# Kernel optimization log

Hardware: AMD Instinct MI355X
Metric: run time of the kernel (lower is better)

## Reference

```python
import jax, jax.numpy as jnp
import numpy as np

V, E, H, A, L = 32000, 512, 1024, 512, 2  # vocab, embed, hidden, attn, n_layers
B, S = 64, 128


def setup_inputs() -> dict:
    key = jax.random.key(0)
    ks = jax.random.split(key, 20)
    sc = 0.02
    inp = {
        "token": jax.random.randint(ks[0], (B,), 0, V),
        "hidden": jax.random.normal(ks[1], (L, B, H), jnp.float32),
        "cell": jax.random.normal(ks[2], (L, B, H), jnp.float32),
        "enc_out": jax.random.normal(ks[3], (S, B, 2 * H), jnp.float32),
        "emb_table": (jax.random.normal(ks[4], (V, E), jnp.float32) * sc).at[0].set(0.0),  # padding_idx=0
        "W_enc": jax.random.normal(ks[5], (A, 2 * H), jnp.float32) * sc,
        "W_dec": jax.random.normal(ks[6], (A, H), jnp.float32) * sc,
        "v_w": jax.random.normal(ks[7], (A,), jnp.float32) * sc,
        "W_ih0": jax.random.normal(ks[8], (4 * H, E + 2 * H), jnp.float32) * sc,
        "W_hh0": jax.random.normal(ks[9], (4 * H, H), jnp.float32) * sc,
        "b_ih0": jax.random.normal(ks[10], (4 * H,), jnp.float32) * sc,
        "b_hh0": jax.random.normal(ks[11], (4 * H,), jnp.float32) * sc,
        "W_ih1": jax.random.normal(ks[12], (4 * H, H), jnp.float32) * sc,
        "W_hh1": jax.random.normal(ks[13], (4 * H, H), jnp.float32) * sc,
        "b_ih1": jax.random.normal(ks[14], (4 * H,), jnp.float32) * sc,
        "b_hh1": jax.random.normal(ks[15], (4 * H,), jnp.float32) * sc,
        "fc_W": jax.random.normal(ks[16], (V, 3 * H), jnp.float32) * sc,
        "fc_b": jax.random.normal(ks[17], (V,), jnp.float32) * sc,
    }
    return inp


def _lstm_cell(x, h, c, W_ih, W_hh, b_ih, b_hh):
    # PyTorch gate order: i, f, g, o
    gates = x @ W_ih.T + h @ W_hh.T + (b_ih + b_hh)  # (B, 4H)
    i, f, g, o = jnp.split(gates, 4, axis=-1)
    i, f, o = jax.nn.sigmoid(i), jax.nn.sigmoid(f), jax.nn.sigmoid(o)
    c_new = f * c + i * jnp.tanh(g)
    h_new = o * jnp.tanh(c_new)
    return h_new, c_new


def reference(token, hidden, cell, enc_out, emb_table, W_enc, W_dec, v_w,
              W_ih0, W_hh0, b_ih0, b_hh0, W_ih1, W_hh1, b_ih1, b_hh1, fc_W, fc_b):
    embedded = emb_table[token]                      # (B, E)
    top = hidden[-1]                                 # (B, H)
    enc_t = jnp.transpose(enc_out, (1, 0, 2))        # (B, S, 2H)
    # additive attention: v . tanh(W_enc enc + W_dec s_t)
    energy = jnp.tanh(jnp.einsum('bsd,ad->bsa', enc_t, W_enc)
                      + (top @ W_dec.T)[:, None, :])  # (B, S, A)
    score = jnp.einsum('bsa,a->bs', energy, v_w)     # (B, S)
    alpha = jax.nn.softmax(score, axis=-1)           # (B, S)
    context = jnp.einsum('bs,bsd->bd', alpha, enc_t)  # (B, 2H)
    x0 = jnp.concatenate([embedded, context], axis=-1)  # (B, E+2H)
    h0, c0 = _lstm_cell(x0, hidden[0], cell[0], W_ih0, W_hh0, b_ih0, b_hh0)
    h1, c1 = _lstm_cell(h0, hidden[1], cell[1], W_ih1, W_hh1, b_ih1, b_hh1)
    logits = jnp.concatenate([h1, context], axis=-1) @ fc_W.T + fc_b  # (B, V)
    new_hidden = jnp.stack([h0, h1], axis=0)
    new_cell = jnp.stack([c0, c1], axis=0)
    return logits, new_hidden, new_cell, alpha
```

## Files before the change

kernel.cpp:

```cpp
#include <hip/hip_runtime.h>
#include <stdint.h>

#define HD    1024
#define BATCH 64
#define SEQ   128
#define AD    512
#define EMBD  512
#define VOCAB 32000

typedef float f32x4 __attribute__((ext_vector_type(4)));
typedef short bf8   __attribute__((ext_vector_type(8)));

#define WS_SCOREP 0
#define WS_DECP   32768
#define WS_G0     65536
#define WS_G1     1114112
#define WS_X0     2162688
#define WS_XFC    2326528
#define WS_H0     2523136

#define OUT_LOGITS 0
#define OUT_HID    2048000
#define OUT_CELL   2179072
#define OUT_ALPHA  2310144

__device__ __forceinline__ short f2bf(float f) {
  uint32_t u = __float_as_uint(f);
  u += 0x7FFF + ((u >> 16) & 1);
  return (short)(u >> 16);
}

__device__ __forceinline__ void store_bf4(short* p, float4 v) {
  short4 s;
  s.x = f2bf(v.x); s.y = f2bf(v.y); s.z = f2bf(v.z); s.w = f2bf(v.w);
  *(short4*)p = s;
}

__global__ __launch_bounds__(256) void k_init(float* __restrict__ ws,
                                              const int* __restrict__ token,
                                              const float* __restrict__ emb) {
  int idx = blockIdx.x * 256 + threadIdx.x;
  int b = idx >> 7, e4 = idx & 127;
  int tok = token[b];
  float4 v = *(const float4*)&emb[(size_t)tok * EMBD + e4 * 4];
  *(float4*)&ws[WS_X0 + (size_t)b * 2560 + e4 * 4] = v;
}

__global__ __launch_bounds__(256) void gemm_thin(
    const float* __restrict__ A, int a_stride,
    const float* __restrict__ Bm,
    float* __restrict__ C, int ldc,
    const float* __restrict__ bias,
    int K_total) {
  __shared__ __align__(16) short As[64][72];
  __shared__ __align__(16) short Bs[64][72];
  const int tid = threadIdx.x;
  const int wave = tid >> 6, lane = tid & 63;
  const int quad = lane >> 4, l16 = lane & 15;
  const int n0 = blockIdx.x * 64;
  const int srow = tid >> 4, sc4 = (tid & 15) * 4;

  f32x4 acc[4];
#pragma unroll
  for (int i = 0; i < 4; ++i) acc[i] = (f32x4){0.f, 0.f, 0.f, 0.f};

  float4 pa[4], pb[4];
#pragma unroll
  for (int p = 0; p < 4; ++p) {
    int row = srow + p * 16;
    pa[p] = *(const float4*)&A[(size_t)row * a_stride + sc4];
    pb[p] = *(const float4*)&Bm[(size_t)(n0 + row) * K_total + sc4];
  }

  for (int kt = 0; kt < K_total; kt += 64) {
#pragma unroll
    for (int p = 0; p < 4; ++p) {
      int row = srow + p * 16;
      store_bf4(&As[row][sc4], pa[p]);
      store_bf4(&Bs[row][sc4], pb[p]);
    }
    __syncthreads();
    if (kt + 64 < K_total) {
      int kn = kt + 64;
#pragma unroll
      for (int p = 0; p < 4; ++p) {
        int row = srow + p * 16;
        pa[p] = *(const float4*)&A[(size_t)row * a_stride + kn + sc4];
        pb[p] = *(const float4*)&Bm[(size_t)(n0 + row) * K_total + kn + sc4];
      }
    }
#pragma unroll
    for (int kk = 0; kk < 64; kk += 32) {
      bf8 af = *(const bf8*)&As[wave * 16 + l16][kk + quad * 8];
#pragma unroll
      for (int ns = 0; ns < 4; ++ns) {
        bf8 bf = *(const bf8*)&Bs[ns * 16 + l16][kk + quad * 8];
        acc[ns] = __builtin_amdgcn_mfma_f32_16x16x32_bf16(af, bf, acc[ns], 0, 0, 0);
      }
    }
    __syncthreads();
  }

#pragma unroll
  for (int ns = 0; ns < 4; ++ns) {
    int n = n0 + ns * 16 + l16;
    float bv = bias ? bias[n] : 0.f;
#pragma unroll
    for (int r = 0; r < 4; ++r) {
      int m = wave * 16 + quad * 4 + r;
      C[(size_t)m * ldc + n] = acc[ns][r] + bv;
    }
  }
}

__global__ __launch_bounds__(256) void gemm2(
    const float* __restrict__ A1, int s1, int K1, const float* __restrict__ B1,
    const float* __restrict__ A2, int s2, int K2, const float* __restrict__ B2,
    float* __restrict__ Cslab, int tiles_pz) {
  __shared__ __align__(16) short As[64][72];
  __shared__ __align__(16) short Bs[64][72];
  const int tid = threadIdx.x;
  const int wave = tid >> 6, lane = tid & 63;
  const int quad = lane >> 4, l16 = lane & 15;
  const int n0 = blockIdx.x * 64;
  const int z = blockIdx.z;
  const int t0 = z * tiles_pz;
  const int srow = tid >> 4, sc4 = (tid & 15) * 4;

  f32x4 acc[4];
#pragma unroll
  for (int i = 0; i < 4; ++i) acc[i] = (f32x4){0.f, 0.f, 0.f, 0.f};

  float4 pa[4], pb[4];
  auto loadAB = [&](int tile) {
    int kv = tile * 64;
    const float* Ap; const float* Bp; int as, ks, ko;
    if (kv < K1) { Ap = A1; Bp = B1; as = s1; ks = K1; ko = kv; }
    else         { Ap = A2; Bp = B2; as = s2; ks = K2; ko = kv - K1; }
#pragma unroll
    for (int p = 0; p < 4; ++p) {
      int row = srow + p * 16;
      pa[p] = *(const float4*)&Ap[(size_t)row * as + ko + sc4];
      pb[p] = *(const float4*)&Bp[(size_t)(n0 + row) * ks + ko + sc4];
    }
  };

  loadAB(t0);
  for (int ti = t0; ti < t0 + tiles_pz; ++ti) {
#pragma unroll
    for (int p = 0; p < 4; ++p) {
      int row = srow + p * 16;
      store_bf4(&As[row][sc4], pa[p]);
      store_bf4(&Bs[row][sc4], pb[p]);
    }
    __syncthreads();
    if (ti + 1 < t0 + tiles_pz) loadAB(ti + 1);
#pragma unroll
    for (int kk = 0; kk < 64; kk += 32) {
      bf8 af = *(const bf8*)&As[wave * 16 + l16][kk + quad * 8];
#pragma unroll
      for (int ns = 0; ns < 4; ++ns) {
        bf8 bf = *(const bf8*)&Bs[ns * 16 + l16][kk + quad * 8];
        acc[ns] = __builtin_amdgcn_mfma_f32_16x16x32_bf16(af, bf, acc[ns], 0, 0, 0);
      }
    }
    __syncthreads();
  }

  float* C = Cslab + (size_t)z * (64 * 4096);
#pragma unroll
  for (int ns = 0; ns < 4; ++ns) {
    int n = n0 + ns * 16 + l16;
#pragma unroll
    for (int r = 0; r < 4; ++r) {
      int m = wave * 16 + quad * 4 + r;
      C[(size_t)m * 4096 + n] = acc[ns][r];
    }
  }
}

__global__ __launch_bounds__(256) void k_attn(
    const float* __restrict__ enc, const float* __restrict__ Wenc,
    const float* __restrict__ dec_proj, const float* __restrict__ vw,
    float* __restrict__ scorep) {
  __shared__ __align__(16) short As[64][72];
  __shared__ __align__(16) short Bs[128][72];
  const int tid = threadIdx.x;
  const int wave = tid >> 6, lane = tid & 63;
  const int quad = lane >> 4, l16 = lane & 15;
  const int mblk = blockIdx.x, nblk = blockIdx.y;
  const int b = mblk >> 1, s0 = (mblk & 1) * 64;
  const int n0 = nblk * 128;
  const size_t abase = ((size_t)s0 * BATCH + b) * 2048;
  const int srow = tid >> 4, sc4 = (tid & 15) * 4;

  f32x4 acc[8];
#pragma unroll
  for (int i = 0; i < 8; ++i) acc[i] = (f32x4){0.f, 0.f, 0.f, 0.f};

  float4 pa[4], pb[8];
  auto loadAB = [&](int kt) {
#pragma unroll
    for (int p = 0; p < 4; ++p) {
      int row = srow + p * 16;
      pa[p] = *(const float4*)&enc[abase + (size_t)row * (BATCH * 2048) + kt + sc4];
    }
#pragma unroll
    for (int p = 0; p < 8; ++p) {
      int row = srow + p * 16;
      pb[p] = *(const float4*)&Wenc[(size_t)(n0 + row) * 2048 + kt + sc4];
    }
  };

  loadAB(0);
  for (int kt = 0; kt < 2048; kt += 64) {
#pragma unroll
    for (int p = 0; p < 4; ++p) store_bf4(&As[srow + p * 16][sc4], pa[p]);
#pragma unroll
    for (int p = 0; p < 8; ++p) store_bf4(&Bs[srow + p * 16][sc4], pb[p]);
    __syncthreads();
    if (kt + 64 < 2048) loadAB(kt + 64);
#pragma unroll
    for (int kk = 0; kk < 64; kk += 32) {
      bf8 af = *(const bf8*)&As[wave * 16 + l16][kk + quad * 8];
#pragma unroll
      for (int ns = 0; ns < 8; ++ns) {
        bf8 bf = *(const bf8*)&Bs[ns * 16 + l16][kk + quad * 8];
        acc[ns] = __builtin_amdgcn_mfma_f32_16x16x32_bf16(af, bf, acc[ns], 0, 0, 0);
      }
    }
    __syncthreads();
  }

  float part[4] = {0.f, 0.f, 0.f, 0.f};
#pragma unroll
  for (int ns = 0; ns < 8; ++ns) {
    int n = n0 + ns * 16 + l16;
    float dp = dec_proj[b * AD + n];
    float vv = vw[n];
#pragma unroll
    for (int r = 0; r < 4; ++r) part[r] += tanhf(acc[ns][r] + dp) * vv;
  }
#pragma unroll
  for (int r = 0; r < 4; ++r) {
    float v = part[r];
    v += __shfl_xor(v, 1);
    v += __shfl_xor(v, 2);
    v += __shfl_xor(v, 4);
    v += __shfl_xor(v, 8);
    if (l16 == 0)
      scorep[nblk * (BATCH * SEQ) + mblk * 64 + wave * 16 + quad * 4 + r] = v;
  }
}

__global__ __launch_bounds__(256) void k_softmax_ctx(
    const float* __restrict__ scorep, const float* __restrict__ enc,
    float* __restrict__ alpha_out, float* __restrict__ x0,
    float* __restrict__ xfc) {
  const int b = blockIdx.x, dchunk = blockIdx.y, t = threadIdx.x;
  __shared__ float al[128];
  __shared__ float buf[128];
  float sv = 0.f;
  if (t < 128) {
    sv = scorep[b * SEQ + t] + scorep[8192 + b * SEQ + t]
       + scorep[16384 + b * SEQ + t] + scorep[24576 + b * SEQ + t];
    buf[t] = sv;
  }
  __syncthreads();
  for (int off = 64; off > 0; off >>= 1) {
    if (t < off) buf[t] = fmaxf(buf[t], buf[t + off]);
    __syncthreads();
  }
  float mx = buf[0];
  __syncthreads();
  float e = 0.f;
  if (t < 128) { e = __expf(sv - mx); buf[t] = e; }
  __syncthreads();
  for (int off = 64; off > 0; off >>= 1) {
    if (t < off) buf[t] += buf[t + off];
    __syncthreads();
  }
  float inv = 1.f / buf[0];
  if (t < 128) {
    float a = e * inv;
    al[t] = a;
    if (dchunk == 0) alpha_out[b * SEQ + t] = a;
  }
  __syncthreads();

  const int d = dchunk * 1024 + t * 4;
  float4 acc = make_float4(0.f, 0.f, 0.f, 0.f);
#pragma unroll 4
  for (int s = 0; s < SEQ; ++s) {
    float4 ev = *(const float4*)&enc[((size_t)s * BATCH + b) * 2048 + d];
    float w = al[s];
    acc.x += w * ev.x; acc.y += w * ev.y;
    acc.z += w * ev.z; acc.w += w * ev.w;
  }
  *(float4*)&x0[(size_t)b * 2560 + 512 + d] = acc;
  *(float4*)&xfc[(size_t)b * 3072 + 1024 + d] = acc;
}

__global__ __launch_bounds__(256) void k_act(
    const float* __restrict__ gslab,
    const float* __restrict__ b_ih, const float* __restrict__ b_hh,
    const float* __restrict__ cell_in,
    float* __restrict__ hid_out, float* __restrict__ cell_out,
    float* __restrict__ hdst, int hstride) {
  int idx = blockIdx.x * 256 + threadIdx.x;
  int b = idx >> 10, n = idx & 1023;
  float gi = b_ih[n]        + b_hh[n];
  float gf = b_ih[1024 + n] + b_hh[1024 + n];
  float gg = b_ih[2048 + n] + b_hh[2048 + n];
  float go = b_ih[3072 + n] + b_hh[3072 + n];
#pragma unroll
  for (int sl = 0; sl < 4; ++sl) {
    const float* g = gslab + (size_t)sl * (64 * 4096) + (size_t)b * 4096;
    gi += g[n];
    gf += g[1024 + n];
    gg += g[2048 + n];
    go += g[3072 + n];
  }
  float i = 1.f / (1.f + __expf(-gi));
  float f = 1.f / (1.f + __expf(-gf));
  float o = 1.f / (1.f + __expf(-go));
  float c = f * cell_in[idx] + i * tanhf(gg);
  float h = o * tanhf(c);
  cell_out[idx] = c;
  hid_out[idx] = h;
  hdst[(size_t)b * hstride + n] = h;
}

extern "C" void kernel_launch(void* const* d_in, const int* in_sizes, int n_in,
                              void* d_out, int out_size, void* d_ws, size_t ws_size,
                              hipStream_t stream) {
  const int*   token  = (const int*)d_in[0];
  const float* hidden = (const float*)d_in[1];
  const float* cell   = (const float*)d_in[2];
  const float* enc    = (const float*)d_in[3];
  const float* emb    = (const float*)d_in[4];
  const float* W_enc  = (const float*)d_in[5];
  const float* W_dec  = (const float*)d_in[6];
  const float* v_w    = (const float*)d_in[7];
  const float* W_ih0  = (const float*)d_in[8];
  const float* W_hh0  = (const float*)d_in[9];
  const float* b_ih0  = (const float*)d_in[10];
  const float* b_hh0  = (const float*)d_in[11];
  const float* W_ih1  = (const float*)d_in[12];
  const float* W_hh1  = (const float*)d_in[13];
  const float* b_ih1  = (const float*)d_in[14];
  const float* b_hh1  = (const float*)d_in[15];
  const float* fc_W   = (const float*)d_in[16];
  const float* fc_b   = (const float*)d_in[17];

  float* out = (float*)d_out;
  float* ws  = (float*)d_ws;

  float* scorep   = ws + WS_SCOREP;
  float* dec_proj = ws + WS_DECP;
  float* gates0   = ws + WS_G0;
  float* gates1   = ws + WS_G1;
  float* x0       = ws + WS_X0;
  float* xfc      = ws + WS_XFC;
  float* h0       = ws + WS_H0;

  k_init<<<32, 256, 0, stream>>>(ws, token, emb);

  gemm_thin<<<dim3(8, 1, 1), 256, 0, stream>>>(
      hidden + BATCH * HD, HD, W_dec, dec_proj, AD, nullptr, 1024);

  k_attn<<<dim3(128, 4), 256, 0, stream>>>(enc, W_enc, dec_proj, v_w, scorep);

  k_softmax_ctx<<<dim3(64, 2), 256, 0, stream>>>(scorep, enc, out + OUT_ALPHA, x0, xfc);

  gemm2<<<dim3(64, 1, 4), 256, 0, stream>>>(
      x0, 2560, 2560, W_ih0, hidden, HD, 1024, W_hh0, gates0, 14);

  k_act<<<256, 256, 0, stream>>>(gates0, b_ih0, b_hh0, cell,
                                 out + OUT_HID, out + OUT_CELL, h0, HD);

  gemm2<<<dim3(64, 1, 4), 256, 0, stream>>>(
      h0, HD, 1024, W_ih1, hidden + BATCH * HD, HD, 1024, W_hh1, gates1, 8);

  k_act<<<256, 256, 0, stream>>>(gates1, b_ih1, b_hh1, cell + BATCH * HD,
                                 out + OUT_HID + BATCH * HD,
                                 out + OUT_CELL + BATCH * HD, xfc, 3072);

  gemm_thin<<<dim3(500, 1, 1), 256, 0, stream>>>(
      xfc, 3072, fc_W, out + OUT_LOGITS, VOCAB, fc_b, 3072);
}
```

Baseline: 768.9 us.

## Split FC GEMM by K and overlap context part with layer-0 gates

Splits the output projection into a context half, computed together with the layer-0 gate GEMM in one launch, and an h1 half computed last that adds the stored partial result. Activations (embedding, context, hidden states, h0/h1) and W_enc are pre-converted to bf16 in workspace so GEMMs load half-width A/B operands. The dec-projection GEMM, embedding gather and conversions are merged into one prep kernel. This fills the GPU better during the small gate GEMM and shortens the serial tail. The cost is extra workspace traffic for the partial logits and the W_enc conversion on every call.

```diff
diff --git a/kernel.cpp b/kernel.cpp
--- a/kernel.cpp
+++ b/kernel.cpp
@@ -15,9 +15,12 @@
 #define WS_DECP   32768
 #define WS_G0     65536
 #define WS_G1     1114112
-#define WS_X0     2162688
-#define WS_XFC    2326528
-#define WS_H0     2523136
+#define WS_LCTX   2162688
+#define WS_X0BF   4210688
+#define WS_XFCBF  4292608
+#define WS_HIDBF  4390912
+#define WS_WENCBF 4456448
+#define WS_H0BF   4980736
 
 #define OUT_LOGITS 0
 #define OUT_HID    2048000
@@ -36,28 +39,14 @@
   *(short4*)p = s;
 }
 
-__global__ __launch_bounds__(256) void k_init(float* __restrict__ ws,
-                                              const int* __restrict__ token,
-                                              const float* __restrict__ emb) {
-  int idx = blockIdx.x * 256 + threadIdx.x;
-  int b = idx >> 7, e4 = idx & 127;
-  int tok = token[b];
-  float4 v = *(const float4*)&emb[(size_t)tok * EMBD + e4 * 4];
-  *(float4*)&ws[WS_X0 + (size_t)b * 2560 + e4 * 4] = v;
-}
-
-__global__ __launch_bounds__(256) void gemm_thin(
-    const float* __restrict__ A, int a_stride,
-    const float* __restrict__ Bm,
-    float* __restrict__ C, int ldc,
-    const float* __restrict__ bias,
-    int K_total) {
-  __shared__ __align__(16) short As[64][72];
-  __shared__ __align__(16) short Bs[64][72];
+__device__ __forceinline__ void gemm_f32A(
+    short (*As)[72], short (*Bs)[72],
+    const float* __restrict__ A, int lda,
+    const float* __restrict__ Bm, int ldb, int K_total, int n0,
+    float* __restrict__ C, int ldc, const float* __restrict__ bias) {
   const int tid = threadIdx.x;
   const int wave = tid >> 6, lane = tid & 63;
   const int quad = lane >> 4, l16 = lane & 15;
-  const int n0 = blockIdx.x * 64;
   const int srow = tid >> 4, sc4 = (tid & 15) * 4;
 
   f32x4 acc[4];
@@ -68,8 +57,8 @@
 #pragma unroll
   for (int p = 0; p < 4; ++p) {
     int row = srow + p * 16;
-    pa[p] = *(const float4*)&A[(size_t)row * a_stride + sc4];
-    pb[p] = *(const float4*)&Bm[(size_t)(n0 + row) * K_total + sc4];
+    pa[p] = *(const float4*)&A[(size_t)row * lda + sc4];
+    pb[p] = *(const float4*)&Bm[(size_t)(n0 + row) * ldb + sc4];
   }
 
   for (int kt = 0; kt < K_total; kt += 64) {
@@ -85,8 +74,8 @@
 #pragma unroll
       for (int p = 0; p < 4; ++p) {
         int row = srow + p * 16;
-        pa[p] = *(const float4*)&A[(size_t)row * a_stride + kn + sc4];
-        pb[p] = *(const float4*)&Bm[(size_t)(n0 + row) * K_total + kn + sc4];
+        pa[p] = *(const float4*)&A[(size_t)row * lda + kn + sc4];
+        pb[p] = *(const float4*)&Bm[(size_t)(n0 + row) * ldb + kn + sc4];
       }
     }
 #pragma unroll
@@ -94,8 +83,8 @@
       bf8 af = *(const bf8*)&As[wave * 16 + l16][kk + quad * 8];
 #pragma unroll
       for (int ns = 0; ns < 4; ++ns) {
-        bf8 bf = *(const bf8*)&Bs[ns * 16 + l16][kk + quad * 8];
-        acc[ns] = __builtin_amdgcn_mfma_f32_16x16x32_bf16(af, bf, acc[ns], 0, 0, 0);
+        bf8 bq = *(const bf8*)&Bs[ns * 16 + l16][kk + quad * 8];
+        acc[ns] = __builtin_amdgcn_mfma_f32_16x16x32_bf16(af, bq, acc[ns], 0, 0, 0);
       }
     }
     __syncthreads();
@@ -113,74 +102,112 @@
   }
 }
 
-__global__ __launch_bounds__(256) void gemm2(
-    const float* __restrict__ A1, int s1, int K1, const float* __restrict__ B1,
-    const float* __restrict__ A2, int s2, int K2, const float* __restrict__ B2,
-    float* __restrict__ Cslab, int tiles_pz) {
-  __shared__ __align__(16) short As[64][72];
-  __shared__ __align__(16) short Bs[64][72];
+__device__ __forceinline__ void gemm_bf16A(
+    short (*As)[72], short (*Bs)[72],
+    const short* __restrict__ A1, int lda1, int K1,
+    const float* __restrict__ B1, int ldb1,
+    const short* __restrict__ A2, int lda2,
+    const float* __restrict__ B2, int ldb2,
+    int t0, int ntiles, int n0,
+    float* __restrict__ C, int ldc,
+    const float* __restrict__ bias,
+    const float* __restrict__ Cadd, int ldadd) {
   const int tid = threadIdx.x;
   const int wave = tid >> 6, lane = tid & 63;
   const int quad = lane >> 4, l16 = lane & 15;
-  const int n0 = blockIdx.x * 64;
-  const int z = blockIdx.z;
-  const int t0 = z * tiles_pz;
-  const int srow = tid >> 4, sc4 = (tid & 15) * 4;
+  const int arow = tid >> 3, ac8 = (tid & 7) * 8;
+  const int brow = tid >> 4, bc4 = (tid & 15) * 4;
 
   f32x4 acc[4];
 #pragma unroll
   for (int i = 0; i < 4; ++i) acc[i] = (f32x4){0.f, 0.f, 0.f, 0.f};
 
-  float4 pa[4], pb[4];
+  bf8 qa[2];
+  float4 pb[4];
   auto loadAB = [&](int tile) {
     int kv = tile * 64;
-    const float* Ap; const float* Bp; int as, ks, ko;
-    if (kv < K1) { Ap = A1; Bp = B1; as = s1; ks = K1; ko = kv; }
-    else         { Ap = A2; Bp = B2; as = s2; ks = K2; ko = kv - K1; }
-#pragma unroll
-    for (int p = 0; p < 4; ++p) {
-      int row = srow + p * 16;
-      pa[p] = *(const float4*)&Ap[(size_t)row * as + ko + sc4];
-      pb[p] = *(const float4*)&Bp[(size_t)(n0 + row) * ks + ko + sc4];
-    }
+    const short* Ap; const float* Bp; int la, lb, ko;
+    if (kv < K1) { Ap = A1; Bp = B1; la = lda1; lb = ldb1; ko = kv; }
+    else         { Ap = A2; Bp = B2; la = lda2; lb = ldb2; ko = kv - K1; }
+#pragma unroll
+    for (int p = 0; p < 2; ++p)
+      qa[p] = *(const bf8*)&Ap[(size_t)(arow + p * 32) * la + ko + ac8];
+#pragma unroll
+    for (int p = 0; p < 4; ++p)
+      pb[p] = *(const float4*)&Bp[(size_t)(n0 + brow + p * 16) * lb + ko + bc4];
   };
 
   loadAB(t0);
-  for (int ti = t0; ti < t0 + tiles_pz; ++ti) {
-#pragma unroll
-    for (int p = 0; p < 4; ++p) {
-      int row = srow + p * 16;
-      store_bf4(&As[row][sc4], pa[p]);
-      store_bf4(&Bs[row][sc4], pb[p]);
-    }
-    __syncthreads();
-    if (ti + 1 < t0 + tiles_pz) loadAB(ti + 1);
+  for (int ti = t0; ti < t0 + ntiles; ++ti) {
+#pragma unroll
+    for (int p = 0; p < 2; ++p) *(bf8*)&As[arow + p * 32][ac8] = qa[p];
+#pragma unroll
+    for (int p = 0; p < 4; ++p) store_bf4(&Bs[brow + p * 16][bc4], pb[p]);
+    __syncthreads();
+    if (ti + 1 < t0 + ntiles) loadAB(ti + 1);
 #pragma unroll
     for (int kk = 0; kk < 64; kk += 32) {
       bf8 af = *(const bf8*)&As[wave * 16 + l16][kk + quad * 8];
 #pragma unroll
       for (int ns = 0; ns < 4; ++ns) {
-        bf8 bf = *(const bf8*)&Bs[ns * 16 + l16][kk + quad * 8];
-        acc[ns] = __builtin_amdgcn_mfma_f32_16x16x32_bf16(af, bf, acc[ns], 0, 0, 0);
+        bf8 bq = *(const bf8*)&Bs[ns * 16 + l16][kk + quad * 8];
+        acc[ns] = __builtin_amdgcn_mfma_f32_16x16x32_bf16(af, bq, acc[ns], 0, 0, 0);
       }
     }
     __syncthreads();
   }
 
-  float* C = Cslab + (size_t)z * (64 * 4096);
 #pragma unroll
   for (int ns = 0; ns < 4; ++ns) {
     int n = n0 + ns * 16 + l16;
+    float bv = bias ? bias[n] : 0.f;
 #pragma unroll
     for (int r = 0; r < 4; ++r) {
       int m = wave * 16 + quad * 4 + r;
-      C[(size_t)m * 4096 + n] = acc[ns][r];
-    }
-  }
+      float v = acc[ns][r] + bv;
+      if (Cadd) v += Cadd[(size_t)m * ldadd + n];
+      C[(size_t)m * ldc + n] = v;
+    }
+  }
+}
+
+__global__ __launch_bounds__(256) void k_prep(
+    float* __restrict__ ws, const int* __restrict__ token,
+    const float* __restrict__ emb, const float* __restrict__ hidden,
+    const float* __restrict__ Wenc, const float* __restrict__ Wdec) {
+  __shared__ __align__(16) short As[64][72];
+  __shared__ __align__(16) short Bs[64][72];
+  const int bx = blockIdx.x, t = threadIdx.x;
+  if (bx < 8) {
+    gemm_f32A(As, Bs, hidden + BATCH * HD, HD, Wdec, HD, 1024, bx * 64,
+              ws + WS_DECP, AD, nullptr);
+    return;
+  }
+  if (bx < 40) {
+    int idx = (bx - 8) * 256 + t;
+    int b = idx >> 7, e4 = (idx & 127) * 4;
+    int tok = token[b];
+    float4 v = *(const float4*)&emb[(size_t)tok * EMBD + e4];
+    store_bf4((short*)(ws + WS_X0BF) + (size_t)b * 2560 + e4, v);
+    return;
+  }
+  if (bx < 168) {
+    int idx = (bx - 40) * 256 + t;
+    float4 v = *(const float4*)&hidden[(size_t)idx * 4];
+    store_bf4((short*)(ws + WS_HIDBF) + (size_t)idx * 4, v);
+    return;
+  }
+  int idx = (bx - 168) * 256 + t;
+  size_t base = (size_t)idx * 8;
+  float4 v0 = *(const float4*)&Wenc[base];
+  float4 v1 = *(const float4*)&Wenc[base + 4];
+  short* dst = (short*)(ws + WS_WENCBF) + base;
+  store_bf4(dst, v0);
+  store_bf4(dst + 4, v1);
 }
 
 __global__ __launch_bounds__(256) void k_attn(
-    const float* __restrict__ enc, const float* __restrict__ Wenc,
+    const float* __restrict__ enc, const short* __restrict__ wencbf,
     const float* __restrict__ dec_proj, const float* __restrict__ vw,
     float* __restrict__ scorep) {
   __shared__ __align__(16) short As[64][72];
@@ -193,12 +220,14 @@
   const int n0 = nblk * 128;
   const size_t abase = ((size_t)s0 * BATCH + b) * 2048;
   const int srow = tid >> 4, sc4 = (tid & 15) * 4;
+  const int brow = tid >> 3, bc8 = (tid & 7) * 8;
 
   f32x4 acc[8];
 #pragma unroll
   for (int i = 0; i < 8; ++i) acc[i] = (f32x4){0.f, 0.f, 0.f, 0.f};
 
-  float4 pa[4], pb[8];
+  float4 pa[4];
+  bf8 qb[4];
   auto loadAB = [&](int kt) {
 #pragma unroll
     for (int p = 0; p < 4; ++p) {
@@ -206,10 +235,8 @@
       pa[p] = *(const float4*)&enc[abase + (size_t)row * (BATCH * 2048) + kt + sc4];
     }
 #pragma unroll
-    for (int p = 0; p < 8; ++p) {
-      int row = srow + p * 16;
-      pb[p] = *(const float4*)&Wenc[(size_t)(n0 + row) * 2048 + kt + sc4];
-    }
+    for (int p = 0; p < 4; ++p)
+      qb[p] = *(const bf8*)&wencbf[(size_t)(n0 + brow + p * 32) * 2048 + kt + bc8];
   };
 
   loadAB(0);
@@ -217,7 +244,7 @@
 #pragma unroll
     for (int p = 0; p < 4; ++p) store_bf4(&As[srow + p * 16][sc4], pa[p]);
 #pragma unroll
-    for (int p = 0; p < 8; ++p) store_bf4(&Bs[srow + p * 16][sc4], pb[p]);
+    for (int p = 0; p < 4; ++p) *(bf8*)&Bs[brow + p * 32][bc8] = qb[p];
     __syncthreads();
     if (kt + 64 < 2048) loadAB(kt + 64);
 #pragma unroll
@@ -225,8 +252,8 @@
       bf8 af = *(const bf8*)&As[wave * 16 + l16][kk + quad * 8];
 #pragma unroll
       for (int ns = 0; ns < 8; ++ns) {
-        bf8 bf = *(const bf8*)&Bs[ns * 16 + l16][kk + quad * 8];
-        acc[ns] = __builtin_amdgcn_mfma_f32_16x16x32_bf16(af, bf, acc[ns], 0, 0, 0);
+        bf8 bq = *(const bf8*)&Bs[ns * 16 + l16][kk + quad * 8];
+        acc[ns] = __builtin_amdgcn_mfma_f32_16x16x32_bf16(af, bq, acc[ns], 0, 0, 0);
       }
     }
     __syncthreads();
@@ -255,8 +282,8 @@
 
 __global__ __launch_bounds__(256) void k_softmax_ctx(
     const float* __restrict__ scorep, const float* __restrict__ enc,
-    float* __restrict__ alpha_out, float* __restrict__ x0,
-    float* __restrict__ xfc) {
+    float* __restrict__ alpha_out, short* __restrict__ x0bf,
+    short* __restrict__ xfcbf) {
   const int b = blockIdx.x, dchunk = blockIdx.y, t = threadIdx.x;
   __shared__ float al[128];
   __shared__ float buf[128];
@@ -297,8 +324,62 @@
     acc.x += w * ev.x; acc.y += w * ev.y;
     acc.z += w * ev.z; acc.w += w * ev.w;
   }
-  *(float4*)&x0[(size_t)b * 2560 + 512 + d] = acc;
-  *(float4*)&xfc[(size_t)b * 3072 + 1024 + d] = acc;
+  store_bf4(&x0bf[(size_t)b * 2560 + 512 + d], acc);
+  store_bf4(&xfcbf[(size_t)b * 3072 + 1024 + d], acc);
+}
+
+__global__ __launch_bounds__(256) void k_big0(
+    float* __restrict__ ws, const float* __restrict__ W_ih0,
+    const float* __restrict__ W_hh0, const float* __restrict__ fc_W) {
+  __shared__ __align__(16) short As[64][72];
+  __shared__ __align__(16) short Bs[64][72];
+  const short* x0bf   = (const short*)(ws + WS_X0BF);
+  const short* hid0bf = (const short*)(ws + WS_HIDBF);
+  const short* xfcbf  = (const short*)(ws + WS_XFCBF);
+  int bx = blockIdx.x;
+  if (bx < 500) {
+    gemm_bf16A(As, Bs,
+               xfcbf + 1024, 3072, 2048, fc_W + 1024, 3072,
+               xfcbf + 1024, 3072, fc_W + 1024, 3072,
+               0, 32, bx * 64,
+               ws + WS_LCTX, VOCAB, nullptr, nullptr, 0);
+  } else {
+    int g = bx - 500;
+    int nblk = g & 63, z = g >> 6;
+    gemm_bf16A(As, Bs,
+               x0bf, 2560, 2560, W_ih0, 2560,
+               hid0bf, 1024, W_hh0, 1024,
+               z * 14, 14, nblk * 64,
+               ws + WS_G0 + (size_t)z * (64 * 4096), 4096, nullptr, nullptr, 0);
+  }
+}
+
+__global__ __launch_bounds__(256) void k_gates1(
+    float* __restrict__ ws, const float* __restrict__ W_ih1,
+    const float* __restrict__ W_hh1) {
+  __shared__ __align__(16) short As[64][72];
+  __shared__ __align__(16) short Bs[64][72];
+  const short* h0bf   = (const short*)(ws + WS_H0BF);
+  const short* hid1bf = (const short*)(ws + WS_HIDBF) + BATCH * HD;
+  int nblk = blockIdx.x & 63, z = blockIdx.x >> 6;
+  gemm_bf16A(As, Bs,
+             h0bf, 1024, 1024, W_ih1, 1024,
+             hid1bf, 1024, W_hh1, 1024,
+             z * 8, 8, nblk * 64,
+             ws + WS_G1 + (size_t)z * (64 * 4096), 4096, nullptr, nullptr, 0);
+}
+
+__global__ __launch_bounds__(256) void k_fc_h1(
+    float* __restrict__ ws, const float* __restrict__ fc_W,
+    const float* __restrict__ fc_b, float* __restrict__ out_logits) {
+  __shared__ __align__(16) short As[64][72];
+  __shared__ __align__(16) short Bs[64][72];
+  const short* xfcbf = (const short*)(ws + WS_XFCBF);
+  gemm_bf16A(As, Bs,
+             xfcbf, 3072, 1024, fc_W, 3072,
+             xfcbf, 3072, fc_W, 3072,
+             0, 16, blockIdx.x * 64,
+             out_logits, VOCAB, fc_b, ws + WS_LCTX, VOCAB);
 }
 
 __global__ __launch_bounds__(256) void k_act(
@@ -306,7 +387,7 @@
     const float* __restrict__ b_ih, const float* __restrict__ b_hh,
     const float* __restrict__ cell_in,
     float* __restrict__ hid_out, float* __restrict__ cell_out,
-    float* __restrict__ hdst, int hstride) {
+    short* __restrict__ hbf, int hstride) {
   int idx = blockIdx.x * 256 + threadIdx.x;
   int b = idx >> 10, n = idx & 1023;
   float gi = b_ih[n]        + b_hh[n];
@@ -328,7 +409,7 @@
   float h = o * tanhf(c);
   cell_out[idx] = c;
   hid_out[idx] = h;
-  hdst[(size_t)b * hstride + n] = h;
+  hbf[(size_t)b * hstride + n] = f2bf(h);
 }
 
 extern "C" void kernel_launch(void* const* d_in, const int* in_sizes, int n_in,
@@ -356,36 +437,27 @@
   float* out = (float*)d_out;
   float* ws  = (float*)d_ws;
 
-  float* scorep   = ws + WS_SCOREP;
-  float* dec_proj = ws + WS_DECP;
-  float* gates0   = ws + WS_G0;
-  float* gates1   = ws + WS_G1;
-  float* x0       = ws + WS_X0;
-  float* xfc      = ws + WS_XFC;
-  float* h0       = ws + WS_H0;
-
-  k_init<<<32, 256, 0, stream>>>(ws, token, emb);
-
-  gemm_thin<<<dim3(8, 1, 1), 256, 0, stream>>>(
-      hidden + BATCH * HD, HD, W_dec, dec_proj, AD, nullptr, 1024);
-
-  k_attn<<<dim3(128, 4), 256, 0, stream>>>(enc, W_enc, dec_proj, v_w, scorep);
-
-  k_softmax_ctx<<<dim3(64, 2), 256, 0, stream>>>(scorep, enc, out + OUT_ALPHA, x0, xfc);
-
-  gemm2<<<dim3(64, 1, 4), 256, 0, stream>>>(
-      x0, 2560, 2560, W_ih0, hidden, HD, 1024, W_hh0, gates0, 14);
-
-  k_act<<<256, 256, 0, stream>>>(gates0, b_ih0, b_hh0, cell,
-                                 out + OUT_HID, out + OUT_CELL, h0, HD);
-
-  gemm2<<<dim3(64, 1, 4), 256, 0, stream>>>(
-      h0, HD, 1024, W_ih1, hidden + BATCH * HD, HD, 1024, W_hh1, gates1, 8);
-
-  k_act<<<256, 256, 0, stream>>>(gates1, b_ih1, b_hh1, cell + BATCH * HD,
+  k_prep<<<680, 256, 0, stream>>>(ws, token, emb, hidden, W_enc, W_dec);
+
+  k_attn<<<dim3(128, 4), 256, 0, stream>>>(
+      enc, (const short*)(ws + WS_WENCBF), ws + WS_DECP, v_w, ws + WS_SCOREP);
+
+  k_softmax_ctx<<<dim3(64, 2), 256, 0, stream>>>(
+      ws + WS_SCOREP, enc, out + OUT_ALPHA,
+      (short*)(ws + WS_X0BF), (short*)(ws + WS_XFCBF));
+
+  k_big0<<<756, 256, 0, stream>>>(ws, W_ih0, W_hh0, fc_W);
+
+  k_act<<<256, 256, 0, stream>>>(ws + WS_G0, b_ih0, b_hh0, cell,
+                                 out + OUT_HID, out + OUT_CELL,
+                                 (short*)(ws + WS_H0BF), HD);
+
+  k_gates1<<<256, 256, 0, stream>>>(ws, W_ih1, W_hh1);
+
+  k_act<<<256, 256, 0, stream>>>(ws + WS_G1, b_ih1, b_hh1, cell + BATCH * HD,
                                  out + OUT_HID + BATCH * HD,
-                                 out + OUT_CELL + BATCH * HD, xfc, 3072);
-
-  gemm_thin<<<dim3(500, 1, 1), 256, 0, stream>>>(
-      xfc, 3072, fc_W, out + OUT_LOGITS, VOCAB, fc_b, 3072);
-}
+                                 out + OUT_CELL + BATCH * HD,
+                                 (short*)(ws + WS_XFCBF), 3072);
+
+  k_fc_h1<<<500, 256, 0, stream>>>(ws, fc_W, fc_b, out + OUT_LOGITS);
+}
```

After: 750.7 us. 2.4% less time.
